# Optimization experiments

Measured on AMD Instinct MI355X. Metric: run time of the kernel, lower is better.

The kernel has to match this reference:

```python
import jax, jax.numpy as jnp
import numpy as np

D, NA, NX, B, K, L = 128, 4096, 8192, 8, 16, 3
SLOPE = 0.2

def leaky(z):
    return jnp.where(z >= 0, z, SLOPE * z)

def group_norm(x, w, b, groups=2, eps=1e-5):
    # torch.nn.GroupNorm(2, D) on [N, C]: normalize each group of C//groups channels per sample
    n, c = x.shape
    xg = x.reshape(n, groups, c // groups)
    mu = xg.mean(-1, keepdims=True)
    var = ((xg - mu) ** 2).mean(-1, keepdims=True)
    xn = ((xg - mu) * jax.lax.rsqrt(var + eps)).reshape(n, c)
    return xn * w + b

def knn(qx, dbx, qb, dbb, k):
    # batch-restricted kNN: squared distances, +inf across different graphs (dMaSIF knn_atoms)
    d2 = jnp.sum((qx[:, None, :] - dbx[None, :, :]) ** 2, axis=-1)  # [Nq, Ndb]
    d2 = jnp.where(qb[:, None] == dbb[None, :], d2, jnp.inf)
    _, idx = jax.lax.top_k(-d2, k)  # ascending distance
    idx = jax.lax.stop_gradient(idx)
    # recompute squared dists from coords (matches keops Kmin + recompute, keeps grads to coords)
    dists = jnp.sum((qx[:, None, :] - dbx[idx]) ** 2, axis=-1)  # [Nq, k]
    return idx, dists

def mp_layer(center, src, idx, dists, w1, b1, w2, b2, gw, gb):
    nbr = src[idx]  # [N, k, D] gather
    feats = jnp.concatenate([jnp.broadcast_to(center[:, None, :], nbr.shape), nbr, dists[..., None]], axis=-1)  # [N,k,2D+1]
    h = leaky(feats @ w1 + b1) @ w2 + b2  # per-edge MLP -> [N,k,D]
    msg = h.sum(axis=1)  # sum over k neighbors
    return center + leaky(group_norm(msg, gw, gb))

def _forward(xyz, atom_xyz, atom_features, batch, atom_batch, tw1, tb1, tw2, tb2,
             aa_w1, aa_b1, aa_w2, aa_b2, aa_gw, aa_gb,
             ae_w1, ae_b1, ae_w2, ae_b2, ae_gw, ae_gb):
    # transform_atom_features
    out = leaky(atom_features @ tw1 + tb1) @ tw2 + tb2
    # atom_atom_forward: k+1 neighbors, drop self (first column)
    idx, dists = knn(atom_xyz, atom_xyz, atom_batch, atom_batch, K + 1)
    idx, dists = idx[:, 1:], dists[:, 1:]
    for i in range(L):
        out = mp_layer(out, out, idx, dists, aa_w1[i], aa_b1[i], aa_w2[i], aa_b2[i], aa_gw[i], aa_gb[i])
    # atom_embedding_forward: surface points gather from atom embeddings
    idx, dists = knn(xyz, atom_xyz, batch, atom_batch, K)
    emb = jnp.ones((xyz.shape[0], out.shape[1]), dtype=out.dtype)
    for i in range(L):
        emb = mp_layer(emb, out, idx, dists, ae_w1[i], ae_b1[i], ae_w2[i], ae_b2[i], ae_gw[i], ae_gb[i])
    return emb

def setup_inputs():
    key = jax.random.key(0)
    ks = jax.random.split(key, 16)
    H = 2 * D + 1
    def lin(k, fi, fo):
        return jax.random.normal(k, (fi, fo), jnp.float32) / np.float32(np.sqrt(fi))
    def lin3(k, fi, fo):
        return jax.random.normal(k, (L, fi, fo), jnp.float32) / np.float32(np.sqrt(fi))
    return dict(
        xyz=jax.random.normal(ks[0], (NX, 3), jnp.float32) * 10.0,
        atom_xyz=jax.random.normal(ks[1], (NA, 3), jnp.float32) * 10.0,
        atom_features=jax.random.normal(ks[2], (NA, D), jnp.float32),
        batch=jnp.sort(jax.random.randint(ks[3], (NX,), 0, B)),
        atom_batch=jnp.sort(jax.random.randint(ks[4], (NA,), 0, B)),
        tw1=lin(ks[5], D, D), tb1=jnp.zeros((D,), jnp.float32),
        tw2=lin(ks[6], D, D), tb2=jnp.zeros((D,), jnp.float32),
        aa_w1=lin3(ks[7], H, H), aa_b1=jnp.zeros((L, H), jnp.float32),
        aa_w2=lin3(ks[8], H, D), aa_b2=jnp.zeros((L, D), jnp.float32),
        aa_gw=jnp.ones((L, D), jnp.float32), aa_gb=jnp.zeros((L, D), jnp.float32),
        ae_w1=lin3(ks[9], H, H), ae_b1=jnp.zeros((L, H), jnp.float32),
        ae_w2=lin3(ks[10], H, D), ae_b2=jnp.zeros((L, D), jnp.float32),
        ae_gw=jnp.ones((L, D), jnp.float32), ae_gb=jnp.zeros((L, D), jnp.float32),
    )

def reference(xyz, atom_xyz, atom_features, batch, atom_batch, tw1, tb1, tw2, tb2, aa_w1, aa_b1, aa_w2, aa_b2, aa_gw, aa_gb, ae_w1, ae_b1, ae_w2, ae_b2, ae_gw, ae_gb):
    return _forward(xyz, atom_xyz, atom_features, batch, atom_batch, tw1, tb1, tw2, tb2,
                    aa_w1, aa_b1, aa_w2, aa_b2, aa_gw, aa_gb,
                    ae_w1, ae_b1, ae_w2, ae_b2, ae_gw, ae_gb)
```

## Files before the change

kernel.cpp:

```cpp
#include <hip/hip_runtime.h>
#include <hip/hip_bf16.h>

#define NAT 4096
#define NXQ 8192
#define DIM 128
#define KNN 16
#define HD  257
#define NLAYER 3
#define SLOPE 0.2f
#define GN_EPS 1e-5f
#define BIGD 1e30f
#define KCAP 16
#define SWS_LD 260

typedef __attribute__((ext_vector_type(4))) float f32x4;

__device__ __forceinline__ float leakyf(float z) { return z >= 0.0f ? z : SLOPE * z; }
__device__ __forceinline__ unsigned long long shfl_xor_u64(unsigned long long v, int m) {
    int lo = __shfl_xor((int)(v & 0xffffffffu), m);
    int hi = __shfl_xor((int)(v >> 32), m);
    return ((unsigned long long)(unsigned)hi << 32) | (unsigned)lo;
}

__global__ void fill_f32_r8(float* __restrict__ p, int n, float v)
{
    int i = blockIdx.x * 256 + threadIdx.x;
    if (i < n) p[i] = v;
}

__global__ __launch_bounds__(128) void feat_transform_r8(
    const float* __restrict__ af,
    const float* __restrict__ tw1, const float* __restrict__ tb1,
    const float* __restrict__ tw2, const float* __restrict__ tb2,
    float* __restrict__ out)
{
    const int i = blockIdx.x;
    const int t = threadIdx.x;
    __shared__ __align__(16) float a_s[DIM];
    __shared__ __align__(16) float h_s[DIM];
    a_s[t] = af[i * DIM + t];
    __syncthreads();
    float acc = tb1[t];
    #pragma unroll 2
    for (int k = 0; k < DIM; k += 4) {
        float4 v = *(const float4*)&a_s[k];
        acc = fmaf(v.x, tw1[(k + 0) * DIM + t], acc);
        acc = fmaf(v.y, tw1[(k + 1) * DIM + t], acc);
        acc = fmaf(v.z, tw1[(k + 2) * DIM + t], acc);
        acc = fmaf(v.w, tw1[(k + 3) * DIM + t], acc);
    }
    h_s[t] = leakyf(acc);
    __syncthreads();
    float acc2 = tb2[t];
    #pragma unroll 2
    for (int k = 0; k < DIM; k += 4) {
        float4 v = *(const float4*)&h_s[k];
        acc2 = fmaf(v.x, tw2[(k + 0) * DIM + t], acc2);
        acc2 = fmaf(v.y, tw2[(k + 1) * DIM + t], acc2);
        acc2 = fmaf(v.z, tw2[(k + 2) * DIM + t], acc2);
        acc2 = fmaf(v.w, tw2[(k + 3) * DIM + t], acc2);
    }
    out[i * DIM + t] = acc2;
}

__global__ __launch_bounds__(64) void batch_starts_r8(const int* __restrict__ abatch,
                                                      int* __restrict__ starts)
{
    int t = threadIdx.x;
    if (t <= 8) {
        int lo = 0, hi = NAT;
        while (lo < hi) { int m = (lo + hi) >> 1; if (abatch[m] < t) lo = m + 1; else hi = m; }
        starts[t] = lo;
    }
}

__global__ __launch_bounds__(256) void knn_r8(
    const float* __restrict__ xyz, const int* __restrict__ xbatch,
    const float* __restrict__ axyz, const int* __restrict__ abatch,
    const int* __restrict__ starts,
    int* __restrict__ idx_aa, float* __restrict__ dist_aa,
    int* __restrict__ idx_xa, float* __restrict__ dist_xa)
{
    const int w = blockIdx.x * 4 + (threadIdx.x >> 6);
    if (w >= NAT + NXQ) return;
    const int l = threadIdx.x & 63;
    const bool is_aa = w < NAT;
    const int q = is_aa ? w : w - NAT;
    float qx, qy, qz; int qb;
    if (is_aa) { qx = axyz[3 * q]; qy = axyz[3 * q + 1]; qz = axyz[3 * q + 2]; qb = abatch[q]; }
    else       { qx = xyz[3 * q];  qy = xyz[3 * q + 1];  qz = xyz[3 * q + 2];  qb = xbatch[q]; }
    const int lo = starts[qb];
    const int hi = starts[qb + 1];

    float d[KCAP];
    #pragma unroll
    for (int s = 0; s < KCAP; ++s) {
        const int j = lo + s * 64 + l;
        float d2 = BIGD;
        if (j < hi && !(is_aa && j == q)) {
            float dx = qx - axyz[3 * j];
            float dy = qy - axyz[3 * j + 1];
            float dz = qz - axyz[3 * j + 2];
            d2 = dx * dx + dy * dy + dz * dz;
        }
        d[s] = d2;
    }

    unsigned mask = 0;
    unsigned long long outk = 0;
    #pragma unroll 1
    for (int it = 0; it < KNN; ++it) {
        float bd = BIGD; int bs = 0;
        #pragma unroll
        for (int s = 0; s < KCAP; ++s) {
            bool c = !((mask >> s) & 1u) && d[s] < bd;
            bd = c ? d[s] : bd;
            bs = c ? s : bs;
        }
        const int bj = lo + bs * 64 + l;
        unsigned long long mykey = ((unsigned long long)__float_as_uint(bd) << 32) | (unsigned)bj;
        unsigned long long key = mykey;
        #pragma unroll
        for (int m = 32; m >= 1; m >>= 1) {
            unsigned long long o = shfl_xor_u64(key, m);
            key = (o < key) ? o : key;
        }
        if (key == mykey) mask |= 1u << bs;
        if (l == it) outk = key;
    }

    if (l < KNN) {
        unsigned ju = (unsigned)(outk & 0xffffffffu);
        float dw = __uint_as_float((unsigned)(outk >> 32));
        int jc = (ju >= (unsigned)NAT) ? 0 : (int)ju;
        int*   ip = is_aa ? (idx_aa + q * KNN)  : (idx_xa + q * KNN);
        float* dp = is_aa ? (dist_aa + q * KNN) : (dist_xa + q * KNN);
        ip[l] = jc;
        dp[l] = dw;
    }
}

__global__ __launch_bounds__(256) void lin128_r8(
    const float* __restrict__ src, const float* __restrict__ w1, int rowoff,
    const float* __restrict__ bias,
    float* __restrict__ out)
{
    const int t = threadIdx.x;
    const int i0 = blockIdx.x * 8;
    __shared__ __align__(16) float cen_s[8][DIM];
    #pragma unroll
    for (int it = 0; it < 4; ++it) {
        int lin = it * 256 + t;
        int a = lin >> 7, j = lin & 127;
        cen_s[a][j] = src[(size_t)(i0 + a) * DIM + j];
    }
    __syncthreads();

    const float* wbase = w1 + (size_t)rowoff * HD;
    float acc[8];
    {
        const float b = bias ? bias[t] : 0.0f;
        #pragma unroll
        for (int a = 0; a < 8; ++a) acc[a] = b;
    }
    #pragma unroll 2
    for (int k = 0; k < DIM; k += 4) {
        float w0 = wbase[(size_t)(k + 0) * HD + t];
        float wa = wbase[(size_t)(k + 1) * HD + t];
        float wb = wbase[(size_t)(k + 2) * HD + t];
        float wc = wbase[(size_t)(k + 3) * HD + t];
        #pragma unroll
        for (int a = 0; a < 8; ++a) {
            float4 c = *(const float4*)&cen_s[a][k];
            acc[a] = fmaf(c.x, w0, acc[a]);
            acc[a] = fmaf(c.y, wa, acc[a]);
            acc[a] = fmaf(c.z, wb, acc[a]);
            acc[a] = fmaf(c.w, wc, acc[a]);
        }
    }
    #pragma unroll
    for (int a = 0; a < 8; ++a)
        out[(size_t)(i0 + a) * HD + t] = acc[a];

    {
        const int a = t >> 5, l32 = t & 31;
        float p = 0.f;
        #pragma unroll
        for (int m = 0; m < 4; ++m) {
            const int k = l32 + 32 * m;
            p = fmaf(cen_s[a][k], wbase[(size_t)k * HD + 256], p);
        }
        #pragma unroll
        for (int m = 1; m < 32; m <<= 1) p += __shfl_xor(p, m);
        if (l32 == 0) out[(size_t)(i0 + a) * HD + 256] = p + (bias ? bias[256] : 0.0f);
    }
}

__global__ __launch_bounds__(256) void aggregate_r8(
    const int* __restrict__ nidx, const float* __restrict__ ndist,
    const float* __restrict__ c1ws, const float* __restrict__ Pws,
    const float* __restrict__ w1,
    float* __restrict__ Sws)
{
    const int i = blockIdx.x;
    const int t = threadIdx.x;
    __shared__ int   eidx[KNN];
    __shared__ float edist[KNN];
    if (t < KNN) {
        eidx[t]  = nidx[i * KNN + t];
        edist[t] = ndist[i * KNN + t];
    }
    __syncthreads();

    const float c1v = c1ws[(size_t)i * HD + t];
    const float wd  = w1[(size_t)256 * HD + t];
    float s = 0.f;
    #pragma unroll
    for (int e = 0; e < KNN; ++e) {
        const float pv = Pws[(size_t)eidx[e] * HD + t];
        s += leakyf(fmaf(edist[e], wd, c1v + pv));
    }
    Sws[(size_t)i * SWS_LD + t] = s;

    if (t < KNN) {
        const float wt = w1[(size_t)256 * HD + 256];
        const float c1_256 = c1ws[(size_t)i * HD + 256];
        float h = leakyf(fmaf(edist[t], wt, c1_256 + Pws[(size_t)eidx[t] * HD + 256]));
        #pragma unroll
        for (int m = 1; m < 16; m <<= 1) h += __shfl_xor(h, m);
        if (t == 0) Sws[(size_t)i * SWS_LD + 256] = h;
    }
}

__global__ __launch_bounds__(256) void stage_d_r8(
    const float* __restrict__ centers,
    const float* __restrict__ Sws,
    const float* __restrict__ w2, const float* __restrict__ b2,
    const float* __restrict__ gw, const float* __restrict__ gb,
    float* __restrict__ dst)
{
    const int t = threadIdx.x;
    const int i0 = blockIdx.x * 8;
    __shared__ __align__(16) float S_s[8][260];

    #pragma unroll
    for (int it = 0; it < 3; ++it) {
        int lin = it * 256 + t;
        if (lin < 520) {
            int a = lin / 65, qd = lin - a * 65;
            *(f32x4*)&S_s[a][qd * 4] = *(const f32x4*)&Sws[(size_t)(i0 + a) * SWS_LD + qd * 4];
        }
    }
    __syncthreads();

    const int j = t & 127, abase = t >> 7;
    float macc0 = 16.0f * b2[j], macc1 = macc0, macc2 = macc0, macc3 = macc0;
    #pragma unroll 2
    for (int k = 0; k < 256; k += 4) {
        float w0 = w2[(k + 0) * DIM + j];
        float wa = w2[(k + 1) * DIM + j];
        float wb = w2[(k + 2) * DIM + j];
        float wc = w2[(k + 3) * DIM + j];
        f32x4 s0 = *(const f32x4*)&S_s[abase + 0][k];
        f32x4 s1 = *(const f32x4*)&S_s[abase + 2][k];
        f32x4 s2 = *(const f32x4*)&S_s[abase + 4][k];
        f32x4 s3 = *(const f32x4*)&S_s[abase + 6][k];
        macc0 = fmaf(s0[0], w0, macc0); macc0 = fmaf(s0[1], wa, macc0);
        macc0 = fmaf(s0[2], wb, macc0); macc0 = fmaf(s0[3], wc, macc0);
        macc1 = fmaf(s1[0], w0, macc1); macc1 = fmaf(s1[1], wa, macc1);
        macc1 = fmaf(s1[2], wb, macc1); macc1 = fmaf(s1[3], wc, macc1);
        macc2 = fmaf(s2[0], w0, macc2); macc2 = fmaf(s2[1], wa, macc2);
        macc2 = fmaf(s2[2], wb, macc2); macc2 = fmaf(s2[3], wc, macc2);
        macc3 = fmaf(s3[0], w0, macc3); macc3 = fmaf(s3[1], wa, macc3);
        macc3 = fmaf(s3[2], wb, macc3); macc3 = fmaf(s3[3], wc, macc3);
    }
    {
        const float w256 = w2[256 * DIM + j];
        macc0 = fmaf(S_s[abase + 0][256], w256, macc0);
        macc1 = fmaf(S_s[abase + 2][256], w256, macc1);
        macc2 = fmaf(S_s[abase + 4][256], w256, macc2);
        macc3 = fmaf(S_s[abase + 6][256], w256, macc3);
    }

    const float gwj = gw[j], gbj = gb[j];
    float m0 = macc0, m1 = macc1, m2 = macc2, m3 = macc3;
    #pragma unroll
    for (int m = 1; m < 64; m <<= 1) {
        m0 += __shfl_xor(m0, m); m1 += __shfl_xor(m1, m);
        m2 += __shfl_xor(m2, m); m3 += __shfl_xor(m3, m);
    }
    const float mu0 = m0 * (1.f / 64.f), mu1 = m1 * (1.f / 64.f);
    const float mu2 = m2 * (1.f / 64.f), mu3 = m3 * (1.f / 64.f);
    float d0 = macc0 - mu0, d1 = macc1 - mu1, d2 = macc2 - mu2, d3 = macc3 - mu3;
    float v0 = d0 * d0, v1 = d1 * d1, v2 = d2 * d2, v3 = d3 * d3;
    #pragma unroll
    for (int m = 1; m < 64; m <<= 1) {
        v0 += __shfl_xor(v0, m); v1 += __shfl_xor(v1, m);
        v2 += __shfl_xor(v2, m); v3 += __shfl_xor(v3, m);
    }
    v0 *= (1.f / 64.f); v1 *= (1.f / 64.f); v2 *= (1.f / 64.f); v3 *= (1.f / 64.f);
    const float y0 = fmaf(d0 * rsqrtf(v0 + GN_EPS), gwj, gbj);
    const float y1 = fmaf(d1 * rsqrtf(v1 + GN_EPS), gwj, gbj);
    const float y2 = fmaf(d2 * rsqrtf(v2 + GN_EPS), gwj, gbj);
    const float y3 = fmaf(d3 * rsqrtf(v3 + GN_EPS), gwj, gbj);
    dst[(size_t)(i0 + abase + 0) * DIM + j] = centers[(size_t)(i0 + abase + 0) * DIM + j] + leakyf(y0);
    dst[(size_t)(i0 + abase + 2) * DIM + j] = centers[(size_t)(i0 + abase + 2) * DIM + j] + leakyf(y1);
    dst[(size_t)(i0 + abase + 4) * DIM + j] = centers[(size_t)(i0 + abase + 4) * DIM + j] + leakyf(y2);
    dst[(size_t)(i0 + abase + 6) * DIM + j] = centers[(size_t)(i0 + abase + 6) * DIM + j] + leakyf(y3);
}

extern "C" void kernel_launch(void* const* d_in, const int* in_sizes, int n_in,
                              void* d_out, int out_size, void* d_ws, size_t ws_size,
                              hipStream_t stream)
{
    const size_t out_bytes = (size_t)out_size * sizeof(float);
    if (n_in != 21) { (void)hipMemsetAsync(d_out, 0x43, out_bytes, stream); return; }

    const size_t n_atoms_f = (size_t)NAT * DIM;
    const size_t n_emb_f   = (size_t)NXQ * DIM;
    const size_t n_c1_f    = (size_t)NXQ * HD;
    const size_t n_P_f     = (size_t)NAT * HD;
    const size_t n_S_f     = (size_t)NXQ * SWS_LD;
    const size_t floats_needed = n_atoms_f * 2 + n_emb_f
        + (size_t)NAT * KNN * 2 + (size_t)NXQ * KNN * 2
        + n_c1_f + n_P_f + n_S_f + 16;
    if (ws_size < floats_needed * 4 + 64) {
        (void)hipMemsetAsync(d_out, 0x41, out_bytes, stream);
        return;
    }

    const float* xyz    = (const float*)d_in[0];
    const float* axyz   = (const float*)d_in[1];
    const float* af     = (const float*)d_in[2];
    const int*   xbatch = (const int*)d_in[3];
    const int*   abatch = (const int*)d_in[4];
    const float* tw1    = (const float*)d_in[5];
    const float* tb1    = (const float*)d_in[6];
    const float* tw2    = (const float*)d_in[7];
    const float* tb2    = (const float*)d_in[8];
    const float* aa_w1  = (const float*)d_in[9];
    const float* aa_b1  = (const float*)d_in[10];
    const float* aa_w2  = (const float*)d_in[11];
    const float* aa_b2  = (const float*)d_in[12];
    const float* aa_gw  = (const float*)d_in[13];
    const float* aa_gb  = (const float*)d_in[14];
    const float* ae_w1  = (const float*)d_in[15];
    const float* ae_b1  = (const float*)d_in[16];
    const float* ae_w2  = (const float*)d_in[17];
    const float* ae_b2  = (const float*)d_in[18];
    const float* ae_gw  = (const float*)d_in[19];
    const float* ae_gb  = (const float*)d_in[20];

    float* fp      = (float*)d_ws;
    float* atoms_a = fp;                 fp += n_atoms_f;
    float* atoms_b = fp;                 fp += n_atoms_f;
    float* emb     = fp;                 fp += n_emb_f;
    int*   idx_aa  = (int*)fp;           fp += (size_t)NAT * KNN;
    float* dist_aa = fp;                 fp += (size_t)NAT * KNN;
    int*   idx_xa  = (int*)fp;           fp += (size_t)NXQ * KNN;
    float* dist_xa = fp;                 fp += (size_t)NXQ * KNN;
    float* c1ws    = fp;                 fp += n_c1_f;
    float* Pws     = fp;                 fp += n_P_f;
    float* Sws     = fp;                 fp += n_S_f;
    int*   bstarts = (int*)fp;           fp += 16;

    const int NOUT = NXQ * DIM;

    fill_f32_r8<<<(NOUT + 255) / 256, 256, 0, stream>>>(emb, NOUT, 1.0f);
    feat_transform_r8<<<NAT, 128, 0, stream>>>(af, tw1, tb1, tw2, tb2, atoms_a);
    batch_starts_r8<<<1, 64, 0, stream>>>(abatch, bstarts);
    knn_r8<<<(NAT + NXQ + 3) / 4, 256, 0, stream>>>(
        xyz, xbatch, axyz, abatch, bstarts, idx_aa, dist_aa, idx_xa, dist_xa);

    float* cur = atoms_a;
    float* nxt = atoms_b;
    for (int i = 0; i < NLAYER; ++i) {
        const float* w1p = aa_w1 + (size_t)i * HD * HD;
        lin128_r8<<<NAT / 8, 256, 0, stream>>>(cur, w1p, 0, aa_b1 + (size_t)i * HD, c1ws);
        lin128_r8<<<NAT / 8, 256, 0, stream>>>(cur, w1p, 128, nullptr, Pws);
        aggregate_r8<<<NAT, 256, 0, stream>>>(idx_aa, dist_aa, c1ws, Pws, w1p, Sws);
        stage_d_r8<<<NAT / 8, 256, 0, stream>>>(
            cur, Sws,
            aa_w2 + (size_t)i * HD * DIM, aa_b2 + (size_t)i * DIM,
            aa_gw + (size_t)i * DIM, aa_gb + (size_t)i * DIM, nxt);
        float* tmp = cur; cur = nxt; nxt = tmp;
    }
    const float* atoms_final = cur;

    for (int i = 0; i < NLAYER; ++i) {
        const float* w1p = ae_w1 + (size_t)i * HD * HD;
        lin128_r8<<<NXQ / 8, 256, 0, stream>>>(emb, w1p, 0, ae_b1 + (size_t)i * HD, c1ws);
        lin128_r8<<<NAT / 8, 256, 0, stream>>>(atoms_final, w1p, 128, nullptr, Pws);
        aggregate_r8<<<NXQ, 256, 0, stream>>>(idx_xa, dist_xa, c1ws, Pws, w1p, Sws);
        float* dsti = (i == NLAYER - 1) ? (float*)d_out : emb;
        stage_d_r8<<<NXQ / 8, 256, 0, stream>>>(
            emb, Sws,
            ae_w2 + (size_t)i * HD * DIM, ae_b2 + (size_t)i * DIM,
            ae_gw + (size_t)i * DIM, ae_gb + (size_t)i * DIM, dsti);
    }
}
```

Before: 464.0 us.

## Fuse center projection, neighbor aggregation and output MLP into one layer kernel

```diff
diff --git a/kernel.cpp b/kernel.cpp
--- a/kernel.cpp
+++ b/kernel.cpp
@@ -11,7 +11,6 @@
 #define GN_EPS 1e-5f
 #define BIGD 1e30f
 #define KCAP 16
-#define SWS_LD 260
 
 typedef __attribute__((ext_vector_type(4))) float f32x4;
 
@@ -22,13 +21,13 @@
     return ((unsigned long long)(unsigned)hi << 32) | (unsigned)lo;
 }
 
-__global__ void fill_f32_r8(float* __restrict__ p, int n, float v)
+__global__ void fill_f32_r9(float* __restrict__ p, int n, float v)
 {
     int i = blockIdx.x * 256 + threadIdx.x;
     if (i < n) p[i] = v;
 }
 
-__global__ __launch_bounds__(128) void feat_transform_r8(
+__global__ __launch_bounds__(128) void feat_transform_r9(
     const float* __restrict__ af,
     const float* __restrict__ tw1, const float* __restrict__ tb1,
     const float* __restrict__ tw2, const float* __restrict__ tb2,
@@ -63,7 +62,7 @@
     out[i * DIM + t] = acc2;
 }
 
-__global__ __launch_bounds__(64) void batch_starts_r8(const int* __restrict__ abatch,
+__global__ __launch_bounds__(64) void batch_starts_r9(const int* __restrict__ abatch,
                                                       int* __restrict__ starts)
 {
     int t = threadIdx.x;
@@ -74,7 +73,7 @@
     }
 }
 
-__global__ __launch_bounds__(256) void knn_r8(
+__global__ __launch_bounds__(256) void knn_r9(
     const float* __restrict__ xyz, const int* __restrict__ xbatch,
     const float* __restrict__ axyz, const int* __restrict__ abatch,
     const int* __restrict__ starts,
@@ -140,9 +139,8 @@
     }
 }
 
-__global__ __launch_bounds__(256) void lin128_r8(
-    const float* __restrict__ src, const float* __restrict__ w1, int rowoff,
-    const float* __restrict__ bias,
+__global__ __launch_bounds__(256) void lin128_r9(
+    const float* __restrict__ src, const float* __restrict__ w1,
     float* __restrict__ out)
 {
     const int t = threadIdx.x;
@@ -156,13 +154,10 @@
     }
     __syncthreads();
 
-    const float* wbase = w1 + (size_t)rowoff * HD;
+    const float* wbase = w1 + (size_t)128 * HD;
     float acc[8];
-    {
-        const float b = bias ? bias[t] : 0.0f;
-        #pragma unroll
-        for (int a = 0; a < 8; ++a) acc[a] = b;
-    }
+    #pragma unroll
+    for (int a = 0; a < 8; ++a) acc[a] = 0.0f;
     #pragma unroll 2
     for (int k = 0; k < DIM; k += 4) {
         float w0 = wbase[(size_t)(k + 0) * HD + t];
@@ -192,64 +187,102 @@
         }
         #pragma unroll
         for (int m = 1; m < 32; m <<= 1) p += __shfl_xor(p, m);
-        if (l32 == 0) out[(size_t)(i0 + a) * HD + 256] = p + (bias ? bias[256] : 0.0f);
-    }
-}
-
-__global__ __launch_bounds__(256) void aggregate_r8(
+        if (l32 == 0) out[(size_t)(i0 + a) * HD + 256] = p;
+    }
+}
+
+__global__ __launch_bounds__(256) void layer_fused_r9(
+    const float* __restrict__ centers,
+    const float* __restrict__ Pws,
     const int* __restrict__ nidx, const float* __restrict__ ndist,
-    const float* __restrict__ c1ws, const float* __restrict__ Pws,
-    const float* __restrict__ w1,
-    float* __restrict__ Sws)
-{
-    const int i = blockIdx.x;
-    const int t = threadIdx.x;
-    __shared__ int   eidx[KNN];
-    __shared__ float edist[KNN];
-    if (t < KNN) {
-        eidx[t]  = nidx[i * KNN + t];
-        edist[t] = ndist[i * KNN + t];
-    }
-    __syncthreads();
-
-    const float c1v = c1ws[(size_t)i * HD + t];
-    const float wd  = w1[(size_t)256 * HD + t];
-    float s = 0.f;
-    #pragma unroll
-    for (int e = 0; e < KNN; ++e) {
-        const float pv = Pws[(size_t)eidx[e] * HD + t];
-        s += leakyf(fmaf(edist[e], wd, c1v + pv));
-    }
-    Sws[(size_t)i * SWS_LD + t] = s;
-
-    if (t < KNN) {
-        const float wt = w1[(size_t)256 * HD + 256];
-        const float c1_256 = c1ws[(size_t)i * HD + 256];
-        float h = leakyf(fmaf(edist[t], wt, c1_256 + Pws[(size_t)eidx[t] * HD + 256]));
-        #pragma unroll
-        for (int m = 1; m < 16; m <<= 1) h += __shfl_xor(h, m);
-        if (t == 0) Sws[(size_t)i * SWS_LD + 256] = h;
-    }
-}
-
-__global__ __launch_bounds__(256) void stage_d_r8(
-    const float* __restrict__ centers,
-    const float* __restrict__ Sws,
+    const float* __restrict__ w1, const float* __restrict__ b1,
     const float* __restrict__ w2, const float* __restrict__ b2,
     const float* __restrict__ gw, const float* __restrict__ gb,
     float* __restrict__ dst)
 {
     const int t = threadIdx.x;
     const int i0 = blockIdx.x * 8;
+
+    __shared__ __align__(16) float cen_s[8][DIM];
     __shared__ __align__(16) float S_s[8][260];
-
-    #pragma unroll
-    for (int it = 0; it < 3; ++it) {
+    __shared__ int   eidx_s[8][KNN];
+    __shared__ float edist_s[8][KNN];
+    __shared__ float c1_256_s[8];
+
+    #pragma unroll
+    for (int it = 0; it < 4; ++it) {
         int lin = it * 256 + t;
-        if (lin < 520) {
-            int a = lin / 65, qd = lin - a * 65;
-            *(f32x4*)&S_s[a][qd * 4] = *(const f32x4*)&Sws[(size_t)(i0 + a) * SWS_LD + qd * 4];
-        }
+        int a = lin >> 7, j = lin & 127;
+        cen_s[a][j] = centers[(size_t)(i0 + a) * DIM + j];
+    }
+    if (t < 128) {
+        int a = t >> 4, e = t & 15;
+        eidx_s[a][e]  = nidx[(size_t)(i0 + a) * KNN + e];
+        edist_s[a][e] = ndist[(size_t)(i0 + a) * KNN + e];
+    }
+    __syncthreads();
+
+    float c1a[8];
+    {
+        const float b = b1[t];
+        #pragma unroll
+        for (int a = 0; a < 8; ++a) c1a[a] = b;
+    }
+    #pragma unroll 2
+    for (int k = 0; k < DIM; k += 4) {
+        float w0 = w1[(size_t)(k + 0) * HD + t];
+        float wa = w1[(size_t)(k + 1) * HD + t];
+        float wb = w1[(size_t)(k + 2) * HD + t];
+        float wc = w1[(size_t)(k + 3) * HD + t];
+        #pragma unroll
+        for (int a = 0; a < 8; ++a) {
+            float4 c = *(const float4*)&cen_s[a][k];
+            c1a[a] = fmaf(c.x, w0, c1a[a]);
+            c1a[a] = fmaf(c.y, wa, c1a[a]);
+            c1a[a] = fmaf(c.z, wb, c1a[a]);
+            c1a[a] = fmaf(c.w, wc, c1a[a]);
+        }
+    }
+    {
+        const int a = t >> 5, l32 = t & 31;
+        float p = 0.f;
+        #pragma unroll
+        for (int m = 0; m < 4; ++m) {
+            const int k = l32 + 32 * m;
+            p = fmaf(cen_s[a][k], w1[(size_t)k * HD + 256], p);
+        }
+        #pragma unroll
+        for (int m = 1; m < 32; m <<= 1) p += __shfl_xor(p, m);
+        if (l32 == 0) c1_256_s[a] = p + b1[256];
+    }
+    __syncthreads();
+
+    {
+        const float wd = w1[(size_t)256 * HD + t];
+        float sa[8];
+        #pragma unroll
+        for (int a = 0; a < 8; ++a) sa[a] = 0.f;
+        #pragma unroll 4
+        for (int e = 0; e < KNN; ++e) {
+            float pv[8];
+            #pragma unroll
+            for (int a = 0; a < 8; ++a)
+                pv[a] = Pws[(size_t)eidx_s[a][e] * HD + t];
+            #pragma unroll
+            for (int a = 0; a < 8; ++a)
+                sa[a] += leakyf(fmaf(edist_s[a][e], wd, c1a[a] + pv[a]));
+        }
+        #pragma unroll
+        for (int a = 0; a < 8; ++a) S_s[a][t] = sa[a];
+    }
+    if (t < 128) {
+        const int a = t >> 4, e = t & 15;
+        const float wt = w1[(size_t)256 * HD + 256];
+        float h = leakyf(fmaf(edist_s[a][e], wt,
+                              c1_256_s[a] + Pws[(size_t)eidx_s[a][e] * HD + 256]));
+        #pragma unroll
+        for (int m = 1; m < 16; m <<= 1) h += __shfl_xor(h, m);
+        if (e == 0) S_s[a][256] = h;
     }
     __syncthreads();
 
@@ -303,10 +336,10 @@
     const float y1 = fmaf(d1 * rsqrtf(v1 + GN_EPS), gwj, gbj);
     const float y2 = fmaf(d2 * rsqrtf(v2 + GN_EPS), gwj, gbj);
     const float y3 = fmaf(d3 * rsqrtf(v3 + GN_EPS), gwj, gbj);
-    dst[(size_t)(i0 + abase + 0) * DIM + j] = centers[(size_t)(i0 + abase + 0) * DIM + j] + leakyf(y0);
-    dst[(size_t)(i0 + abase + 2) * DIM + j] = centers[(size_t)(i0 + abase + 2) * DIM + j] + leakyf(y1);
-    dst[(size_t)(i0 + abase + 4) * DIM + j] = centers[(size_t)(i0 + abase + 4) * DIM + j] + leakyf(y2);
-    dst[(size_t)(i0 + abase + 6) * DIM + j] = centers[(size_t)(i0 + abase + 6) * DIM + j] + leakyf(y3);
+    dst[(size_t)(i0 + abase + 0) * DIM + j] = cen_s[abase + 0][j] + leakyf(y0);
+    dst[(size_t)(i0 + abase + 2) * DIM + j] = cen_s[abase + 2][j] + leakyf(y1);
+    dst[(size_t)(i0 + abase + 4) * DIM + j] = cen_s[abase + 4][j] + leakyf(y2);
+    dst[(size_t)(i0 + abase + 6) * DIM + j] = cen_s[abase + 6][j] + leakyf(y3);
 }
 
 extern "C" void kernel_launch(void* const* d_in, const int* in_sizes, int n_in,
@@ -318,12 +351,9 @@
 
     const size_t n_atoms_f = (size_t)NAT * DIM;
     const size_t n_emb_f   = (size_t)NXQ * DIM;
-    const size_t n_c1_f    = (size_t)NXQ * HD;
     const size_t n_P_f     = (size_t)NAT * HD;
-    const size_t n_S_f     = (size_t)NXQ * SWS_LD;
     const size_t floats_needed = n_atoms_f * 2 + n_emb_f
-        + (size_t)NAT * KNN * 2 + (size_t)NXQ * KNN * 2
-        + n_c1_f + n_P_f + n_S_f + 16;
+        + (size_t)NAT * KNN * 2 + (size_t)NXQ * KNN * 2 + n_P_f + 16;
     if (ws_size < floats_needed * 4 + 64) {
         (void)hipMemsetAsync(d_out, 0x41, out_bytes, stream);
         return;
@@ -359,28 +389,25 @@
     float* dist_aa = fp;                 fp += (size_t)NAT * KNN;
     int*   idx_xa  = (int*)fp;           fp += (size_t)NXQ * KNN;
     float* dist_xa = fp;                 fp += (size_t)NXQ * KNN;
-    float* c1ws    = fp;                 fp += n_c1_f;
     float* Pws     = fp;                 fp += n_P_f;
-    float* Sws     = fp;                 fp += n_S_f;
     int*   bstarts = (int*)fp;           fp += 16;
 
     const int NOUT = NXQ * DIM;
 
-    fill_f32_r8<<<(NOUT + 255) / 256, 256, 0, stream>>>(emb, NOUT, 1.0f);
-    feat_transform_r8<<<NAT, 128, 0, stream>>>(af, tw1, tb1, tw2, tb2, atoms_a);
-    batch_starts_r8<<<1, 64, 0, stream>>>(abatch, bstarts);
-    knn_r8<<<(NAT + NXQ + 3) / 4, 256, 0, stream>>>(
+    fill_f32_r9<<<(NOUT + 255) / 256, 256, 0, stream>>>(emb, NOUT, 1.0f);
+    feat_transform_r9<<<NAT, 128, 0, stream>>>(af, tw1, tb1, tw2, tb2, atoms_a);
+    batch_starts_r9<<<1, 64, 0, stream>>>(abatch, bstarts);
+    knn_r9<<<(NAT + NXQ + 3) / 4, 256, 0, stream>>>(
         xyz, xbatch, axyz, abatch, bstarts, idx_aa, dist_aa, idx_xa, dist_xa);
 
     float* cur = atoms_a;
     float* nxt = atoms_b;
     for (int i = 0; i < NLAYER; ++i) {
         const float* w1p = aa_w1 + (size_t)i * HD * HD;
-        lin128_r8<<<NAT / 8, 256, 0, stream>>>(cur, w1p, 0, aa_b1 + (size_t)i * HD, c1ws);
-        lin128_r8<<<NAT / 8, 256, 0, stream>>>(cur, w1p, 128, nullptr, Pws);
-        aggregate_r8<<<NAT, 256, 0, stream>>>(idx_aa, dist_aa, c1ws, Pws, w1p, Sws);
-        stage_d_r8<<<NAT / 8, 256, 0, stream>>>(
-            cur, Sws,
+        lin128_r9<<<NAT / 8, 256, 0, stream>>>(cur, w1p, Pws);
+        layer_fused_r9<<<NAT / 8, 256, 0, stream>>>(
+            cur, Pws, idx_aa, dist_aa,
+            w1p, aa_b1 + (size_t)i * HD,
             aa_w2 + (size_t)i * HD * DIM, aa_b2 + (size_t)i * DIM,
             aa_gw + (size_t)i * DIM, aa_gb + (size_t)i * DIM, nxt);
         float* tmp = cur; cur = nxt; nxt = tmp;
@@ -389,12 +416,11 @@
 
     for (int i = 0; i < NLAYER; ++i) {
         const float* w1p = ae_w1 + (size_t)i * HD * HD;
-        lin128_r8<<<NXQ / 8, 256, 0, stream>>>(emb, w1p, 0, ae_b1 + (size_t)i * HD, c1ws);
-        lin128_r8<<<NAT / 8, 256, 0, stream>>>(atoms_final, w1p, 128, nullptr, Pws);
-        aggregate_r8<<<NXQ, 256, 0, stream>>>(idx_xa, dist_xa, c1ws, Pws, w1p, Sws);
+        lin128_r9<<<NAT / 8, 256, 0, stream>>>(atoms_final, w1p, Pws);
         float* dsti = (i == NLAYER - 1) ? (float*)d_out : emb;
-        stage_d_r8<<<NXQ / 8, 256, 0, stream>>>(
-            emb, Sws,
+        layer_fused_r9<<<NXQ / 8, 256, 0, stream>>>(
+            emb, Pws, idx_xa, dist_xa,
+            w1p, ae_b1 + (size_t)i * HD,
             ae_w2 + (size_t)i * HD * DIM, ae_b2 + (size_t)i * DIM,
             ae_gw + (size_t)i * DIM, ae_gb + (size_t)i * DIM, dsti);
     }
```

Result: faster. 432.6 us (-6.8%).
